# Kernel optimization log

Measured on AMD Instinct MI355X. Metric: run time of the kernel, lower is better.

## Reference

```python
import jax, jax.numpy as jnp
import numpy as np

B, H, W, C, NH, WS = 64, 56, 56, 128, 4, 7
N = H * W


def setup_inputs() -> dict:
    key = jax.random.key(0)
    ks = jax.random.split(key, 6)
    return {
        "x": jax.random.normal(ks[0], (B, N, C), jnp.float32),
        "w_qkv": jax.random.normal(ks[1], (3 * C, C), jnp.float32) * 0.02,
        "w_lim": jax.random.normal(ks[2], (C, 1, 3, 3), jnp.float32) * 0.02,
        "b_lim": jax.random.normal(ks[3], (C,), jnp.float32) * 0.02,
        "w_proj": jax.random.normal(ks[4], (C, C), jnp.float32) * 0.02,
        "b_proj": jax.random.normal(ks[5], (C,), jnp.float32) * 0.02,
        "H": H,
        "W": W,
    }


def reference(x, w_qkv, w_lim, b_lim, w_proj, b_proj, H, W):
    Bq, Nq, Cq = x.shape
    ws, nh = WS, NH
    hd = Cq // nh
    hg, wg = H // ws, W // ws  # 8, 8 -- no padding needed at these shapes
    scale = hd ** -0.5

    qkv = x @ w_qkv.T                      # (B, N, 3C)
    q, k, v = jnp.split(qkv, 3, axis=-1)

    def img2win(t):
        # (B,N,C) -> (B, hg*wg, nh, ws*ws, hd)
        t = t.reshape(Bq, hg, ws, wg, ws, Cq).transpose(0, 1, 3, 2, 4, 5)
        return t.reshape(Bq, hg * wg, ws * ws, nh, hd).transpose(0, 1, 3, 2, 4)

    qw, kw, vw = img2win(q), img2win(k), img2win(v)

    # LIM: depthwise 3x3 conv on shape-integrated V (win2img(img2win(v)) == v as NCHW)
    v_img = v.reshape(Bq, H, W, Cq).transpose(0, 3, 1, 2)     # (B,C,H,W)
    v_lim = jax.lax.conv_general_dilated(
        v_img, w_lim, window_strides=(1, 1), padding='SAME',
        dimension_numbers=('NCHW', 'OIHW', 'NCHW'), feature_group_count=Cq)
    v_lim = v_lim + b_lim[None, :, None, None]
    v_lim = v_lim.reshape(Bq, Cq, Nq).transpose(0, 2, 1)      # (B,N,C)

    # windowed attention: g = window index, n = head
    attn = jax.nn.softmax(
        jnp.einsum('bgnqd,bgnkd->bgnqk', qw, kw) * scale, axis=-1)
    out = jnp.einsum('bgnqk,bgnkd->bgnqd', attn, vw)          # (B,g,nh,ws*ws,hd)

    # merge windows back: (B,g,nh,ws*ws,hd) -> (B,N,C)
    out = out.transpose(0, 1, 3, 2, 4).reshape(Bq, hg, wg, ws, ws, Cq)
    out = out.transpose(0, 1, 3, 2, 4, 5).reshape(Bq, Nq, Cq)

    out = out + v_lim
    return out @ w_proj.T + b_proj
```

## Files before the change

### kernel.cpp

```cpp
#include <hip/hip_runtime.h>
#include <cstdint>

#define B_   64
#define H_   56
#define W_   56
#define C_   128
#define WSZ  7
#define TT   49
#define NN   3136
#define MM   (B_ * NN)
#define SCALE 0.17677669529663687f

typedef short bf16x8 __attribute__((ext_vector_type(8)));
typedef float f32x4  __attribute__((ext_vector_type(4)));
typedef unsigned short u16;

__device__ __forceinline__ float bf2f(u16 u) {
    return __uint_as_float(((unsigned int)u) << 16);
}
__device__ __forceinline__ u16 f2bf(float f) {
    unsigned int u = __float_as_uint(f);
    u += 0x7FFFu + ((u >> 16) & 1u);
    return (u16)(u >> 16);
}

__global__ __launch_bounds__(256) void ka_fused(
    const float* __restrict__ x, const float* __restrict__ wqkv,
    u16* __restrict__ vout, float* __restrict__ out)
{
    __shared__ u16 arena[4][64][136];
    u16* ps_ = &arena[1][0][0];

    const int t   = threadIdx.x;
    const int blk = blockIdx.x;
    const int b_  = blk >> 6, wr = blk & 63;
    const int qy  = wr >> 3, qx = wr & 7;
    const int wave = t >> 6, lane = t & 63, lr = lane & 15, quad = lane >> 4;

    for (int i = t; i < 64 * 32; i += 256) {
        int tok = i >> 5, c4 = (i & 31) * 4;
        ushort4 u4 = {0, 0, 0, 0};
        if (tok < TT) {
            int hh = qy * WSZ + tok / WSZ, ww = qx * WSZ + tok % WSZ;
            float4 f = *(const float4*)&x[((size_t)b_ * NN + hh * W_ + ww) * C_ + c4];
            u4.x = f2bf(f.x); u4.y = f2bf(f.y);
            u4.z = f2bf(f.z); u4.w = f2bf(f.w);
        }
        *(ushort4*)&arena[0][tok][c4] = u4;
    }
    __syncthreads();

    for (int ch = 0; ch < 3; ch++) {
        const float mul = (ch == 0) ? SCALE : 1.0f;
        u16 (*dst)[136] = arena[1 + ch];
#pragma unroll
        for (int half = 0; half < 2; half++) {
            const float* wrow =
                &wqkv[(size_t)(ch * 128 + half * 64 + wave * 16 + lr) * C_];
            f32x4 acc[4];
#pragma unroll
            for (int mi = 0; mi < 4; mi++) acc[mi] = {0.f, 0.f, 0.f, 0.f};
#pragma unroll
            for (int kk = 0; kk < 4; kk++) {
                float4 f0 = *(const float4*)&wrow[kk * 32 + quad * 8];
                float4 f1 = *(const float4*)&wrow[kk * 32 + quad * 8 + 4];
                bf16x8 bfr;
                bfr[0] = (short)f2bf(f0.x); bfr[1] = (short)f2bf(f0.y);
                bfr[2] = (short)f2bf(f0.z); bfr[3] = (short)f2bf(f0.w);
                bfr[4] = (short)f2bf(f1.x); bfr[5] = (short)f2bf(f1.y);
                bfr[6] = (short)f2bf(f1.z); bfr[7] = (short)f2bf(f1.w);
#pragma unroll
                for (int mi = 0; mi < 4; mi++) {
                    bf16x8 afr = *(const bf16x8*)&arena[0][mi * 16 + lr][kk * 32 + quad * 8];
                    acc[mi] = __builtin_amdgcn_mfma_f32_16x16x32_bf16(
                        afr, bfr, acc[mi], 0, 0, 0);
                }
            }
#pragma unroll
            for (int mi = 0; mi < 4; mi++) {
#pragma unroll
                for (int r = 0; r < 4; r++) {
                    int tok = mi * 16 + quad * 4 + r;
                    int col = half * 64 + wave * 16 + lr;
                    u16 bv = f2bf(acc[mi][r] * mul);
                    dst[tok][col] = bv;
                    if (ch == 2 && tok < TT) {
                        int hh2 = qy * WSZ + tok / WSZ;
                        int ww2 = qx * WSZ + tok % WSZ;
                        vout[((size_t)b_ * NN + hh2 * W_ + ww2) * C_ + col] = bv;
                    }
                }
            }
        }
    }
    __syncthreads();

    const int h = wave;
    bf16x8 qf[4], kf[4];
#pragma unroll
    for (int mi = 0; mi < 4; mi++) {
        qf[mi] = *(const bf16x8*)&arena[1][mi * 16 + lr][h * 32 + quad * 8];
        kf[mi] = *(const bf16x8*)&arena[2][mi * 16 + lr][h * 32 + quad * 8];
    }
    __syncthreads();

    f32x4 s[4][4];
#pragma unroll
    for (int mi = 0; mi < 4; mi++)
#pragma unroll
        for (int nj = 0; nj < 4; nj++) s[mi][nj] = {0.f, 0.f, 0.f, 0.f};
#pragma unroll
    for (int mi = 0; mi < 4; mi++)
#pragma unroll
        for (int nj = 0; nj < 4; nj++)
            s[mi][nj] = __builtin_amdgcn_mfma_f32_16x16x32_bf16(
                qf[mi], kf[nj], s[mi][nj], 0, 0, 0);

    if (lr >= 1) {
#pragma unroll
        for (int mi = 0; mi < 4; mi++)
#pragma unroll
            for (int r = 0; r < 4; r++) s[mi][3][r] = -1e30f;
    }

    float rsum[4][4];
#pragma unroll
    for (int mi = 0; mi < 4; mi++) {
#pragma unroll
        for (int r = 0; r < 4; r++) {
            float mx = fmaxf(fmaxf(s[mi][0][r], s[mi][1][r]),
                             fmaxf(s[mi][2][r], s[mi][3][r]));
#pragma unroll
            for (int off = 1; off < 16; off <<= 1)
                mx = fmaxf(mx, __shfl_xor(mx, off));
            float sum = 0.f;
#pragma unroll
            for (int nj = 0; nj < 4; nj++) {
                float p = __expf(s[mi][nj][r] - mx);
                s[mi][nj][r] = p;
                sum += p;
            }
#pragma unroll
            for (int off = 1; off < 16; off <<= 1)
                sum += __shfl_xor(sum, off);
            rsum[mi][r] = sum;
        }
    }

#pragma unroll
    for (int mi = 0; mi < 4; mi++)
#pragma unroll
        for (int nj = 0; nj < 4; nj++)
#pragma unroll
            for (int r = 0; r < 4; r++)
                ps_[((h * 64) + mi * 16 + quad * 4 + r) * 64 + nj * 16 + lr] =
                    f2bf(s[mi][nj][r]);

    f32x4 o[4][2];
#pragma unroll
    for (int mi = 0; mi < 4; mi++)
#pragma unroll
        for (int nv = 0; nv < 2; nv++) o[mi][nv] = {0.f, 0.f, 0.f, 0.f};

#pragma unroll
    for (int kt = 0; kt < 2; kt++) {
        bf16x8 pf[4];
#pragma unroll
        for (int mi = 0; mi < 4; mi++)
            pf[mi] = *(const bf16x8*)&ps_[((h * 64) + mi * 16 + lr) * 64 +
                                          kt * 32 + quad * 8];
        bf16x8 vf[2];
#pragma unroll
        for (int nv = 0; nv < 2; nv++) {
            bf16x8 tmp;
#pragma unroll
            for (int jj = 0; jj < 8; jj++)
                tmp[jj] = (short)arena[3][kt * 32 + quad * 8 + jj][h * 32 + nv * 16 + lr];
            vf[nv] = tmp;
        }
#pragma unroll
        for (int mi = 0; mi < 4; mi++)
#pragma unroll
            for (int nv = 0; nv < 2; nv++)
                o[mi][nv] = __builtin_amdgcn_mfma_f32_16x16x32_bf16(
                    pf[mi], vf[nv], o[mi][nv], 0, 0, 0);
    }

#pragma unroll
    for (int mi = 0; mi < 4; mi++) {
#pragma unroll
        for (int r = 0; r < 4; r++) {
            int i = mi * 16 + quad * 4 + r;
            if (i < TT) {
                int hh = qy * WSZ + i / WSZ, ww = qx * WSZ + i % WSZ;
                size_t orow = (size_t)b_ * NN + hh * W_ + ww;
                float inv = 1.f / rsum[mi][r];
#pragma unroll
                for (int nv = 0; nv < 2; nv++)
                    out[orow * C_ + h * 32 + nv * 16 + lr] = o[mi][nv][r] * inv;
            }
        }
    }
}

__global__ __launch_bounds__(256) void kb_lim(
    const u16* __restrict__ v, const float* __restrict__ wlim,
    const float* __restrict__ blim, float* __restrict__ out)
{
    const int t   = threadIdx.x;
    const int pos = blockIdx.x * 16 + (t >> 4);
    const int c0  = (t & 15) * 8;
    const int b_  = pos / NN;
    const int rem = pos - b_ * NN;
    const int hh  = rem / W_;
    const int ww  = rem - hh * W_;

    float w72[72];
    {
        const float* wp = &wlim[c0 * 9];
#pragma unroll
        for (int i = 0; i < 18; i++) {
            float4 f = *(const float4*)&wp[i * 4];
            w72[i * 4 + 0] = f.x; w72[i * 4 + 1] = f.y;
            w72[i * 4 + 2] = f.z; w72[i * 4 + 3] = f.w;
        }
    }
    float acc[8];
    {
        float4 b0 = *(const float4*)&blim[c0];
        float4 b1 = *(const float4*)&blim[c0 + 4];
        acc[0] = b0.x; acc[1] = b0.y; acc[2] = b0.z; acc[3] = b0.w;
        acc[4] = b1.x; acc[5] = b1.y; acc[6] = b1.z; acc[7] = b1.w;
    }

    const u16* vbase = &v[(size_t)b_ * NN * C_ + c0];
#pragma unroll
    for (int dy = -1; dy <= 1; dy++) {
        int y = hh + dy;
        bool yok = (unsigned)y < (unsigned)H_;
#pragma unroll
        for (int dx = -1; dx <= 1; dx++) {
            int x2 = ww + dx;
            bool ok = yok && ((unsigned)x2 < (unsigned)W_);
            bf16x8 vv = {0, 0, 0, 0, 0, 0, 0, 0};
            if (ok) vv = *(const bf16x8*)&vbase[(size_t)(y * W_ + x2) * C_];
            const int tap = (dy + 1) * 3 + (dx + 1);
#pragma unroll
            for (int j = 0; j < 8; j++)
                acc[j] += bf2f((u16)vv[j]) * w72[j * 9 + tap];
        }
    }

    float* op = &out[(size_t)pos * C_ + c0];
    float4 o0 = *(const float4*)&op[0];
    float4 o1 = *(const float4*)&op[4];
    o0.x += acc[0]; o0.y += acc[1]; o0.z += acc[2]; o0.w += acc[3];
    o1.x += acc[4]; o1.y += acc[5]; o1.z += acc[6]; o1.w += acc[7];
    *(float4*)&op[0] = o0;
    *(float4*)&op[4] = o1;
}

__global__ __launch_bounds__(256) void kc_proj(
    float* __restrict__ y, const float* __restrict__ wproj,
    const float* __restrict__ bproj)
{
    __shared__ u16 As[128][72];
    __shared__ u16 Ws[128][72];
    const int t    = threadIdx.x;
    const int m0   = blockIdx.x * 128;
    const int wave = t >> 6, lane = t & 63, lr = lane & 15, quad = lane >> 4;
    const int wm = (wave >> 1) * 64, wn = (wave & 1) * 64;

    f32x4 acc[4][4];
#pragma unroll
    for (int mi = 0; mi < 4; mi++)
#pragma unroll
        for (int ni = 0; ni < 4; ni++) acc[mi][ni] = {0.f, 0.f, 0.f, 0.f};

#pragma unroll
    for (int kt = 0; kt < 2; kt++) {
        const int k0 = kt * 64;
#pragma unroll
        for (int p = 0; p < 8; p++) {
            int e   = p * 256 + t;
            int row = e >> 4;
            int col = (e & 15) * 4;
            float4 fa = *(const float4*)&y[(size_t)(m0 + row) * C_ + k0 + col];
            ushort4 ua;
            ua.x = f2bf(fa.x); ua.y = f2bf(fa.y);
            ua.z = f2bf(fa.z); ua.w = f2bf(fa.w);
            *(ushort4*)&As[row][col] = ua;
            float4 fw = *(const float4*)&wproj[(size_t)row * C_ + k0 + col];
            ushort4 uw;
            uw.x = f2bf(fw.x); uw.y = f2bf(fw.y);
            uw.z = f2bf(fw.z); uw.w = f2bf(fw.w);
            *(ushort4*)&Ws[row][col] = uw;
        }
        __syncthreads();
#pragma unroll
        for (int kk = 0; kk < 2; kk++) {
            bf16x8 a[4], b[4];
#pragma unroll
            for (int mi = 0; mi < 4; mi++)
                a[mi] = *(const bf16x8*)&As[wm + mi * 16 + lr][kk * 32 + quad * 8];
#pragma unroll
            for (int ni = 0; ni < 4; ni++)
                b[ni] = *(const bf16x8*)&Ws[wn + ni * 16 + lr][kk * 32 + quad * 8];
#pragma unroll
            for (int mi = 0; mi < 4; mi++)
#pragma unroll
                for (int ni = 0; ni < 4; ni++)
                    acc[mi][ni] = __builtin_amdgcn_mfma_f32_16x16x32_bf16(
                        a[mi], b[ni], acc[mi][ni], 0, 0, 0);
        }
        if (kt == 0) __syncthreads();
    }

#pragma unroll
    for (int mi = 0; mi < 4; mi++) {
#pragma unroll
        for (int r = 0; r < 4; r++) {
            int m = m0 + wm + mi * 16 + quad * 4 + r;
#pragma unroll
            for (int ni = 0; ni < 4; ni++) {
                int c = wn + ni * 16 + lr;
                y[(size_t)m * C_ + c] = acc[mi][ni][r] + bproj[c];
            }
        }
    }
}

extern "C" void kernel_launch(void* const* d_in, const int* in_sizes, int n_in,
                              void* d_out, int out_size, void* d_ws, size_t ws_size,
                              hipStream_t stream)
{
    const float* x     = (const float*)d_in[0];
    const float* wqkv  = (const float*)d_in[1];
    const float* wlim  = (const float*)d_in[2];
    const float* blim  = (const float*)d_in[3];
    const float* wproj = (const float*)d_in[4];
    const float* bproj = (const float*)d_in[5];
    float* out = (float*)d_out;
    u16*   v   = (u16*)d_ws;

    ka_fused<<<dim3(B_ * 64), 256, 0, stream>>>(x, wqkv, v, out);
    kb_lim  <<<dim3(MM / 16), 256, 0, stream>>>(v, wlim, blim, out);
    kc_proj <<<dim3(MM / 128), 256, 0, stream>>>(out, wproj, bproj);
}
```

Before: 454.8 us.

## Shrink LDS arena by reusing x tile buffer for Q and padding P/V strides

Cuts the shared-memory footprint from four 64x136 buffers to about three by computing K and V first, holding Q in registers, then overwriting the x tile with scaled Q after a barrier. Launch bounds now request 3 blocks per SM to use the extra occupancy the smaller LDS allows. The P scratch row stride is padded to 68 and the V stride to 138 to cut bank conflicts, with P reads split into two 4-element loads. In exchange it adds a barrier and keeps more accumulator registers live during the Q GEMM, which may cause spills under the tighter register budget.

```diff
diff --git a/kernel.cpp b/kernel.cpp
--- a/kernel.cpp
+++ b/kernel.cpp
@@ -12,6 +12,7 @@
 #define SCALE 0.17677669529663687f
 
 typedef short bf16x8 __attribute__((ext_vector_type(8)));
+typedef short bf16x4 __attribute__((ext_vector_type(4)));
 typedef float f32x4  __attribute__((ext_vector_type(4)));
 typedef unsigned short u16;
 
@@ -24,12 +25,15 @@
     return (u16)(u >> 16);
 }
 
-__global__ __launch_bounds__(256) void ka_fused(
+__global__ __launch_bounds__(256, 3) void ka_fused(
     const float* __restrict__ x, const float* __restrict__ wqkv,
     u16* __restrict__ vout, float* __restrict__ out)
 {
-    __shared__ u16 arena[4][64][136];
-    u16* ps_ = &arena[1][0][0];
+    __shared__ u16 lds[26240];
+    u16 (*xq)[136] = (u16(*)[136])&lds[0];
+    u16 (*ks)[136] = (u16(*)[136])&lds[8704];
+    u16 (*vs)[138] = (u16(*)[138])&lds[17408];
+    u16* ps_ = &lds[0];
 
     const int t   = threadIdx.x;
     const int blk = blockIdx.x;
@@ -46,13 +50,15 @@
             u4.x = f2bf(f.x); u4.y = f2bf(f.y);
             u4.z = f2bf(f.z); u4.w = f2bf(f.w);
         }
-        *(ushort4*)&arena[0][tok][c4] = u4;
+        *(ushort4*)&xq[tok][c4] = u4;
     }
     __syncthreads();
 
-    for (int ch = 0; ch < 3; ch++) {
-        const float mul = (ch == 0) ? SCALE : 1.0f;
-        u16 (*dst)[136] = arena[1 + ch];
+#pragma unroll
+    for (int cc = 0; cc < 2; cc++) {
+        const int ch = 1 + cc;
+        u16* dstbase = cc ? &vs[0][0] : &ks[0][0];
+        const int dstride = cc ? 138 : 136;
 #pragma unroll
         for (int half = 0; half < 2; half++) {
             const float* wrow =
@@ -71,7 +77,7 @@
                 bfr[6] = (short)f2bf(f1.z); bfr[7] = (short)f2bf(f1.w);
 #pragma unroll
                 for (int mi = 0; mi < 4; mi++) {
-                    bf16x8 afr = *(const bf16x8*)&arena[0][mi * 16 + lr][kk * 32 + quad * 8];
+                    bf16x8 afr = *(const bf16x8*)&xq[mi * 16 + lr][kk * 32 + quad * 8];
                     acc[mi] = __builtin_amdgcn_mfma_f32_16x16x32_bf16(
                         afr, bfr, acc[mi], 0, 0, 0);
                 }
@@ -82,9 +88,9 @@
                 for (int r = 0; r < 4; r++) {
                     int tok = mi * 16 + quad * 4 + r;
                     int col = half * 64 + wave * 16 + lr;
-                    u16 bv = f2bf(acc[mi][r] * mul);
-                    dst[tok][col] = bv;
-                    if (ch == 2 && tok < TT) {
+                    u16 bv = f2bf(acc[mi][r]);
+                    dstbase[tok * dstride + col] = bv;
+                    if (cc == 1 && tok < TT) {
                         int hh2 = qy * WSZ + tok / WSZ;
                         int ww2 = qx * WSZ + tok % WSZ;
                         vout[((size_t)b_ * NN + hh2 * W_ + ww2) * C_ + col] = bv;
@@ -93,14 +99,50 @@
             }
         }
     }
+
+    f32x4 qacc[2][4];
+#pragma unroll
+    for (int half = 0; half < 2; half++)
+#pragma unroll
+        for (int mi = 0; mi < 4; mi++) qacc[half][mi] = {0.f, 0.f, 0.f, 0.f};
+#pragma unroll
+    for (int half = 0; half < 2; half++) {
+        const float* wrow = &wqkv[(size_t)(half * 64 + wave * 16 + lr) * C_];
+#pragma unroll
+        for (int kk = 0; kk < 4; kk++) {
+            float4 f0 = *(const float4*)&wrow[kk * 32 + quad * 8];
+            float4 f1 = *(const float4*)&wrow[kk * 32 + quad * 8 + 4];
+            bf16x8 bfr;
+            bfr[0] = (short)f2bf(f0.x); bfr[1] = (short)f2bf(f0.y);
+            bfr[2] = (short)f2bf(f0.z); bfr[3] = (short)f2bf(f0.w);
+            bfr[4] = (short)f2bf(f1.x); bfr[5] = (short)f2bf(f1.y);
+            bfr[6] = (short)f2bf(f1.z); bfr[7] = (short)f2bf(f1.w);
+#pragma unroll
+            for (int mi = 0; mi < 4; mi++) {
+                bf16x8 afr = *(const bf16x8*)&xq[mi * 16 + lr][kk * 32 + quad * 8];
+                qacc[half][mi] = __builtin_amdgcn_mfma_f32_16x16x32_bf16(
+                    afr, bfr, qacc[half][mi], 0, 0, 0);
+            }
+        }
+    }
+    __syncthreads();
+
+#pragma unroll
+    for (int half = 0; half < 2; half++)
+#pragma unroll
+        for (int mi = 0; mi < 4; mi++)
+#pragma unroll
+            for (int r = 0; r < 4; r++)
+                xq[mi * 16 + quad * 4 + r][half * 64 + wave * 16 + lr] =
+                    f2bf(qacc[half][mi][r] * SCALE);
     __syncthreads();
 
     const int h = wave;
     bf16x8 qf[4], kf[4];
 #pragma unroll
     for (int mi = 0; mi < 4; mi++) {
-        qf[mi] = *(const bf16x8*)&arena[1][mi * 16 + lr][h * 32 + quad * 8];
-        kf[mi] = *(const bf16x8*)&arena[2][mi * 16 + lr][h * 32 + quad * 8];
+        qf[mi] = *(const bf16x8*)&xq[mi * 16 + lr][h * 32 + quad * 8];
+        kf[mi] = *(const bf16x8*)&ks[mi * 16 + lr][h * 32 + quad * 8];
     }
     __syncthreads();
 
@@ -153,7 +195,7 @@
         for (int nj = 0; nj < 4; nj++)
 #pragma unroll
             for (int r = 0; r < 4; r++)
-                ps_[((h * 64) + mi * 16 + quad * 4 + r) * 64 + nj * 16 + lr] =
+                ps_[((h * 64) + mi * 16 + quad * 4 + r) * 68 + nj * 16 + lr] =
                     f2bf(s[mi][nj][r]);
 
     f32x4 o[4][2];
@@ -166,16 +208,22 @@
     for (int kt = 0; kt < 2; kt++) {
         bf16x8 pf[4];
 #pragma unroll
-        for (int mi = 0; mi < 4; mi++)
-            pf[mi] = *(const bf16x8*)&ps_[((h * 64) + mi * 16 + lr) * 64 +
-                                          kt * 32 + quad * 8];
+        for (int mi = 0; mi < 4; mi++) {
+            const u16* pp = &ps_[((h * 64) + mi * 16 + lr) * 68 + kt * 32 + quad * 8];
+            bf16x4 lo = *(const bf16x4*)&pp[0];
+            bf16x4 hi = *(const bf16x4*)&pp[4];
+            bf16x8 f;
+            f[0] = lo[0]; f[1] = lo[1]; f[2] = lo[2]; f[3] = lo[3];
+            f[4] = hi[0]; f[5] = hi[1]; f[6] = hi[2]; f[7] = hi[3];
+            pf[mi] = f;
+        }
         bf16x8 vf[2];
 #pragma unroll
         for (int nv = 0; nv < 2; nv++) {
             bf16x8 tmp;
 #pragma unroll
             for (int jj = 0; jj < 8; jj++)
-                tmp[jj] = (short)arena[3][kt * 32 + quad * 8 + jj][h * 32 + nv * 16 + lr];
+                tmp[jj] = (short)vs[kt * 32 + quad * 8 + jj][h * 32 + nv * 16 + lr];
             vf[nv] = tmp;
         }
 #pragma unroll
```

Measured after the change: 440.1 us. -3.2%, faster.
